# Optimization experiments

Hardware: AMD Instinct MI355X
Metric: run time of the kernel (lower is better)

Reference implementation:

```python
import jax, jax.numpy as jnp
import numpy as np

BATCH = 8
IMG = 224
PATCH = 16
IN_CH = 8
D_MODEL = 768
DEPTH = 4
D_INNER = 2 * D_MODEL          # 1536
D_STATE = 16
DT_RANK = D_MODEL // 16        # 48
D_CONV = 4
NUM_CLASSES = 1000
EPS = 1e-5


def setup_inputs() -> dict:
    key = jax.random.key(0)
    ks = jax.random.split(key, 16)
    g = lambda i, shape, s=0.02: jax.random.normal(ks[i], shape, jnp.float32) * s
    L = DEPTH
    inp = {}
    inp['x'] = jax.random.normal(ks[0], (BATCH, IN_CH, IMG, IMG), jnp.float32)
    # patch embed: Conv3d(1, D, (1,p,p)) == shared 2D conv applied to every channel
    inp['patch_w'] = g(1, (D_MODEL, PATCH, PATCH))
    inp['patch_b'] = jnp.zeros((D_MODEL,), jnp.float32)
    inp['channel_embed'] = g(2, (IN_CH, D_MODEL))
    # per-block params (stacked over depth)
    inp['norm_w'] = jnp.ones((L, D_MODEL), jnp.float32)
    inp['norm_b'] = jnp.zeros((L, D_MODEL), jnp.float32)
    inp['in_proj_w'] = g(3, (L, 2 * D_INNER, D_MODEL))
    inp['conv_w'] = g(4, (L, D_INNER, D_CONV), 0.1)
    inp['conv_b'] = jnp.zeros((L, D_INNER), jnp.float32)
    inp['x_proj_w'] = g(5, (L, DT_RANK + 2 * D_STATE, D_INNER))
    inp['dt_proj_w'] = g(6, (L, D_INNER, DT_RANK), 0.1)
    inp['dt_proj_b'] = jnp.full((L, D_INNER), -4.6, jnp.float32)  # softplus^-1(0.01)
    inp['A_log'] = jnp.tile(jnp.log(jnp.arange(1, D_STATE + 1, dtype=jnp.float32)), (L, D_INNER, 1))
    inp['D_param'] = jnp.ones((L, D_INNER), jnp.float32)
    inp['ssm_norm_w'] = jnp.ones((L, D_INNER), jnp.float32)
    inp['ssm_norm_b'] = jnp.zeros((L, D_INNER), jnp.float32)
    inp['out_proj_w'] = g(7, (L, D_MODEL, D_INNER), 0.02 / np.sqrt(L))
    # final norm + classification head
    inp['norm_f_w'] = jnp.ones((D_MODEL,), jnp.float32)
    inp['norm_f_b'] = jnp.zeros((D_MODEL,), jnp.float32)
    inp['head_w'] = g(8, (NUM_CLASSES, D_MODEL))
    inp['head_b'] = jnp.zeros((NUM_CLASSES,), jnp.float32)
    return inp


def _ln(x, w, b):
    mu = x.mean(-1, keepdims=True)
    var = ((x - mu) ** 2).mean(-1, keepdims=True)
    return (x - mu) * jax.lax.rsqrt(var + EPS) * w + b


def _silu(x):
    return x * jax.nn.sigmoid(x)


def _mamba(h, ipw, cw, cb, xpw, dtw, dtb, Alog, Dp, snw, snb, opw):
    # h: [B, L, D_MODEL]
    B, Lseq, _ = h.shape
    xz = jnp.einsum('bld,ed->ble', h, ipw)               # [B, L, 2*di]
    x, z = jnp.split(xz, 2, axis=-1)
    # causal depthwise conv1d along L (kernel D_CONV)
    xp = jnp.pad(x, ((0, 0), (D_CONV - 1, 0), (0, 0)))
    xc = cb + sum(xp[:, k:k + Lseq, :] * cw[:, k] for k in range(D_CONV))
    x = _silu(xc)
    dbc = jnp.einsum('bld,ed->ble', x, xpw)              # [B, L, dt_rank+2N]
    dt_r = dbc[..., :DT_RANK]
    Bm = dbc[..., DT_RANK:DT_RANK + D_STATE]
    Cm = dbc[..., DT_RANK + D_STATE:]
    dt = jax.nn.softplus(jnp.einsum('blr,dr->bld', dt_r, dtw) + dtb)  # [B, L, di]
    A = -jnp.exp(Alog)                                    # [di, N]

    def step(hstate, t):
        dt_t, B_t, C_t, x_t = t                           # [B,di],[B,N],[B,N],[B,di]
        dA = jnp.exp(dt_t[..., None] * A)                 # [B, di, N]
        hstate = dA * hstate + (dt_t * x_t)[..., None] * B_t[:, None, :]
        y = jnp.einsum('bdn,bn->bd', hstate, C_t)
        return hstate, y

    h0 = jnp.zeros((B, D_INNER, D_STATE), x.dtype)
    xs = (dt.transpose(1, 0, 2), Bm.transpose(1, 0, 2),
          Cm.transpose(1, 0, 2), x.transpose(1, 0, 2))
    _, ys = jax.lax.scan(step, h0, xs)                    # [L, B, di]
    y = ys.transpose(1, 0, 2) + Dp * x
    y = _ln(y, snw, snb)                                  # norm-after-SSM
    y = y * _silu(z)
    return jnp.einsum('ble,de->bld', y, opw)


def reference(x, patch_w, patch_b, channel_embed, norm_w, norm_b, in_proj_w,
              conv_w, conv_b, x_proj_w, dt_proj_w, dt_proj_b, A_log, D_param,
              ssm_norm_w, ssm_norm_b, out_proj_w, norm_f_w, norm_f_b,
              head_w, head_b):
    B, C, H, W = x.shape
    hg, wg = H // PATCH, W // PATCH
    # shared-filter patch embed per channel: [B,C,hg,wg,D]
    xp = x.reshape(B, C, hg, PATCH, wg, PATCH)
    emb = jnp.einsum('bchpwq,dpq->bchwd', xp, patch_w) + patch_b
    emb = emb + channel_embed[None, :, None, None, :]
    # Channel-First scan order -> token order (h, w, C): [B, hg*wg*C, D]
    tok = emb.transpose(0, 2, 3, 1, 4).reshape(B, hg * wg * C, D_MODEL)

    hidden, residual = tok, None
    for i in range(DEPTH):
        residual = hidden if residual is None else residual + hidden
        hn = _ln(residual, norm_w[i], norm_b[i])
        hidden = _mamba(hn, in_proj_w[i], conv_w[i], conv_b[i], x_proj_w[i],
                        dt_proj_w[i], dt_proj_b[i], A_log[i], D_param[i],
                        ssm_norm_w[i], ssm_norm_b[i], out_proj_w[i])
    residual = residual + hidden
    hf = _ln(residual, norm_f_w, norm_f_b)
    pooled = hf.mean(axis=1)                              # mean pooling head
    return pooled @ head_w.T + head_b
```

## Files before the change

### kernel.cpp

```cpp
#include <hip/hip_runtime.h>
#include <hip/hip_bf16.h>

typedef __hip_bfloat16 bf16;
typedef __attribute__((ext_vector_type(8))) short short8;
typedef __attribute__((ext_vector_type(4))) float float4v;

#define BATCH 8
#define SEQ   1568
#define M_TOK (BATCH*SEQ)
#define DM    768
#define DI    1536
#define XZW   3072
#define DS    16
#define DTR   48
#define NCLS  1000
#define LAYERS 4
#define CHUNK 112
#define NCH   14
#define DBCW  128

__device__ __forceinline__ float b2f(bf16 v){ return __bfloat162float(v); }
__device__ __forceinline__ bf16  f2b(float v){ return __float2bfloat16(v); }
__device__ __forceinline__ float us2f(unsigned short u){
    unsigned v = ((unsigned)u) << 16; float f; __builtin_memcpy(&f, &v, 4); return f;
}
__device__ __forceinline__ void gload_lds16(const void* g, void* l){
    __builtin_amdgcn_global_load_lds(
        (const __attribute__((address_space(1))) void*)g,
        (__attribute__((address_space(3))) void*)l, 16, 0, 0);
}
template<int CTRL>
__device__ __forceinline__ float dpp_add(float p){
    int pi; __builtin_memcpy(&pi, &p, 4);
    int mi = __builtin_amdgcn_update_dpp(pi, pi, CTRL, 0xF, 0xF, false);
    float m; __builtin_memcpy(&m, &mi, 4);
    return p + m;
}

__global__ void detect_dtype(const unsigned short* __restrict__ probe, unsigned* __restrict__ flag)
{
    if (threadIdx.x == 0 && blockIdx.x == 0) flag[0] = (probe[0] == 0) ? 1u : 0u;
}

struct CvtArgs {
    const void* src[21];
    void*       dst[21];
    int         n[21];
    unsigned    f32mask;
    int         total;
};

__global__ __launch_bounds__(256)
void convert_all(CvtArgs a, const unsigned* __restrict__ flag)
{
    int idx = blockIdx.x*256 + threadIdx.x;
    if (idx >= a.total) return;
    int i = 0, base = 0;
    while (idx >= base + a.n[i]) { base += a.n[i]; ++i; }
    int j = idx - base;
    bool in_f32 = flag[0] != 0;
    if ((a.f32mask >> i) & 1u) {
        float v = in_f32 ? ((const float*)a.src[i])[j] : b2f(((const bf16*)a.src[i])[j]);
        ((float*)a.dst[i])[j] = v;
    } else {
        bf16 v = in_f32 ? f2b(((const float*)a.src[i])[j]) : ((const bf16*)a.src[i])[j];
        ((bf16*)a.dst[i])[j] = v;
    }
}

__global__ __launch_bounds__(256)
void pad_dtw(const bf16* __restrict__ src, bf16* __restrict__ dst)
{
    int idx = blockIdx.x*256 + threadIdx.x;
    if (idx >= LAYERS*DI*64) return;
    int l = idx / (DI*64);
    int d = (idx / 64) % DI;
    int c = idx % 64;
    dst[idx] = (c < DTR) ? src[((size_t)l*DI + d)*DTR + c] : f2b(0.f);
}

__global__ __launch_bounds__(256)
void gather_patches(const bf16* __restrict__ x, bf16* __restrict__ Ap, int b0)
{
    size_t idx = (size_t)blockIdx.x*256 + threadIdx.x;
    int i = (int)(idx & 255);
    int m = (int)(idx >> 8);
    int b = b0 + m / SEQ, s = m % SEQ;
    int hw = s >> 3, c = s & 7;
    int h = hw / 14, w = hw % 14;
    int p = i >> 4, q = i & 15;
    Ap[idx] = x[(((size_t)(b*8 + c)*224) + h*16 + p)*224 + w*16 + q];
}

__global__ __launch_bounds__(256)
void gemm_mfma(const bf16* __restrict__ A, int lda,
               const bf16* __restrict__ W, int ldw,
               float* __restrict__ Cf, bf16* __restrict__ Cb, int ldc,
               const float* __restrict__ bias, const float* __restrict__ chan,
               int M, int N, int K, int epi)
{
    __shared__ short As[128*40];
    __shared__ short Bs[128*40];
    int tid  = threadIdx.x;
    int m0   = blockIdx.x*128, n0 = blockIdx.y*128;
    int lane = tid & 63, wv = tid >> 6;
    int wm = (wv >> 1)*64, wn = (wv & 1)*64;
    int l15 = lane & 15, quad = lane >> 4;

    float4v acc[4][4];
    #pragma unroll
    for (int i = 0; i < 4; ++i)
        #pragma unroll
        for (int j = 0; j < 4; ++j) acc[i][j] = (float4v){0.f,0.f,0.f,0.f};

    const short8 zv8 = {0,0,0,0,0,0,0,0};
    for (int k0 = 0; k0 < K; k0 += 32) {
        #pragma unroll
        for (int u = 0; u < 2; ++u) {
            int c   = tid*2 + u;
            int row = c >> 2, ch = c & 3;
            bool kok = (k0 + ch*8 + 8) <= K;
            short8 va = (kok && m0 + row < M)
                ? *(const short8*)((const short*)A + (size_t)(m0+row)*lda + k0 + ch*8) : zv8;
            *(short8*)(As + row*40 + ch*8) = va;
            short8 vb = (kok && n0 + row < N)
                ? *(const short8*)((const short*)W + (size_t)(n0+row)*ldw + k0 + ch*8) : zv8;
            *(short8*)(Bs + row*40 + ch*8) = vb;
        }
        __syncthreads();
        short8 av[4], bv[4];
        #pragma unroll
        for (int i = 0; i < 4; ++i) av[i] = *(const short8*)(As + (wm + i*16 + l15)*40 + quad*8);
        #pragma unroll
        for (int j = 0; j < 4; ++j) bv[j] = *(const short8*)(Bs + (wn + j*16 + l15)*40 + quad*8);
        #pragma unroll
        for (int i = 0; i < 4; ++i)
            #pragma unroll
            for (int j = 0; j < 4; ++j)
                acc[i][j] = __builtin_amdgcn_mfma_f32_16x16x32_bf16(av[i], bv[j], acc[i][j], 0, 0, 0);
        __syncthreads();
    }

    #pragma unroll
    for (int i = 0; i < 4; ++i) {
        #pragma unroll
        for (int j = 0; j < 4; ++j) {
            int gn = n0 + wn + j*16 + l15;
            if (gn >= N) continue;
            #pragma unroll
            for (int r = 0; r < 4; ++r) {
                int gm = m0 + wm + i*16 + quad*4 + r;
                if (gm >= M) continue;
                float v = acc[i][j][r];
                size_t off = (size_t)gm*ldc + gn;
                if (epi == 0)      Cb[off] = f2b(v);
                else if (epi == 1) {
                    v += bias[gn];
                    v = (v > 20.f) ? v : log1pf(__expf(v));
                    Cb[off] = f2b(v);
                }
                else if (epi == 2) Cf[off] += v;
                else               Cf[off] = v + bias[gn] + chan[(size_t)(gm & 7)*N + gn];
            }
        }
    }
}

__global__ __launch_bounds__(256)
void gemm_mfma_fast(const bf16* __restrict__ A, int lda,
                    const bf16* __restrict__ W, int ldw,
                    float* __restrict__ Cf, bf16* __restrict__ Cb, int ldc,
                    const float* __restrict__ bias, const float* __restrict__ chan,
                    int N, int K, int epi)
{
    __shared__ short As[128*32];
    __shared__ short Bs[128*32];
    int tid  = threadIdx.x;
    int m0   = blockIdx.x*128, n0 = blockIdx.y*128;
    int lane = tid & 63, wv = tid >> 6;
    int wm = (wv >> 1)*64, wn = (wv & 1)*64;
    int l15 = lane & 15, quad = lane >> 4;

    int srow = (lane >> 2);
    int skof = (lane & 3) * 8;

    float4v acc[4][4];
    #pragma unroll
    for (int i = 0; i < 4; ++i)
        #pragma unroll
        for (int j = 0; j < 4; ++j) acc[i][j] = (float4v){0.f,0.f,0.f,0.f};

    const short* Ab = (const short*)A;
    const short* Wb = (const short*)W;

    for (int k0 = 0; k0 < K; k0 += 32) {
        #pragma unroll
        for (int u = 0; u < 2; ++u) {
            int c = wv*2 + u;
            int row = c*16 + srow;
            gload_lds16(Ab + (size_t)(m0+row)*lda + k0 + skof, As + c*512);
            gload_lds16(Wb + (size_t)(n0+row)*ldw + k0 + skof, Bs + c*512);
        }
        __syncthreads();
        short8 av[4], bv[4];
        #pragma unroll
        for (int i = 0; i < 4; ++i) av[i] = *(const short8*)(As + (wm + i*16 + l15)*32 + quad*8);
        #pragma unroll
        for (int j = 0; j < 4; ++j) bv[j] = *(const short8*)(Bs + (wn + j*16 + l15)*32 + quad*8);
        #pragma unroll
        for (int i = 0; i < 4; ++i)
            #pragma unroll
            for (int j = 0; j < 4; ++j)
                acc[i][j] = __builtin_amdgcn_mfma_f32_16x16x32_bf16(av[i], bv[j], acc[i][j], 0, 0, 0);
        __syncthreads();
    }

    #pragma unroll
    for (int i = 0; i < 4; ++i) {
        #pragma unroll
        for (int j = 0; j < 4; ++j) {
            int gn = n0 + wn + j*16 + l15;
            #pragma unroll
            for (int r = 0; r < 4; ++r) {
                int gm = m0 + wm + i*16 + quad*4 + r;
                float v = acc[i][j][r];
                size_t off = (size_t)gm*ldc + gn;
                if (epi == 0)      Cb[off] = f2b(v);
                else if (epi == 1) {
                    v += bias[gn];
                    v = (v > 20.f) ? v : log1pf(__expf(v));
                    Cb[off] = f2b(v);
                }
                else if (epi == 2) Cf[off] += v;
                else               Cf[off] = v + bias[gn] + chan[(size_t)(gm & 7)*N + gn];
            }
        }
    }
}

__global__ __launch_bounds__(256)
void ln768(const float* __restrict__ X, const float* __restrict__ w,
           const float* __restrict__ bb, bf16* __restrict__ out)
{
    __shared__ float red[8];
    size_t t = blockIdx.x;
    const float* x = X + t*DM;
    float v[3]; float s = 0.f, s2 = 0.f;
    #pragma unroll
    for (int r = 0; r < 3; ++r) {
        v[r] = x[threadIdx.x + 256*r];
        s += v[r]; s2 += v[r]*v[r];
    }
    #pragma unroll
    for (int o = 32; o; o >>= 1) { s += __shfl_down(s, o, 64); s2 += __shfl_down(s2, o, 64); }
    if ((threadIdx.x & 63) == 0) { red[threadIdx.x >> 6] = s; red[(threadIdx.x >> 6) + 4] = s2; }
    __syncthreads();
    s  = red[0]+red[1]+red[2]+red[3];
    s2 = red[4]+red[5]+red[6]+red[7];
    float mu  = s * (1.f/DM);
    float inv = rsqrtf(fmaxf(s2*(1.f/DM) - mu*mu, 0.f) + 1e-5f);
    #pragma unroll
    for (int r = 0; r < 3; ++r) {
        int i = threadIdx.x + 256*r;
        out[t*DM + i] = f2b((v[r]-mu)*inv*w[i] + bb[i]);
    }
}

__global__ __launch_bounds__(256)
void conv_silu(const bf16* __restrict__ xz, const float* __restrict__ cw,
               const float* __restrict__ cb, bf16* __restrict__ xc)
{
    size_t idx = (size_t)blockIdx.x*256 + threadIdx.x;
    int dv = (int)(idx % (DI/8));
    int m  = (int)(idx / (DI/8));
    int b = m / SEQ, t = m % SEQ;
    int d = dv*8;

    float4v cwq[8];
    #pragma unroll
    for (int j = 0; j < 8; ++j) cwq[j] = *(const float4v*)(cw + (size_t)(d+j)*4);

    float acc[8];
    #pragma unroll
    for (int j = 0; j < 8; ++j) acc[j] = cb[d+j];

    #pragma unroll
    for (int k = 0; k < 4; ++k) {
        int tt = t + k - 3;
        if (tt >= 0) {
            short8 v = *(const short8*)((const short*)xz + (size_t)(b*SEQ + tt)*XZW + d);
            #pragma unroll
            for (int j = 0; j < 8; ++j)
                acc[j] += us2f((unsigned short)v[j]) * cwq[j][k];
        }
    }
    short8 o;
    #pragma unroll
    for (int j = 0; j < 8; ++j) {
        float sig = 1.f/(1.f + __expf(-acc[j]));
        bf16 r = f2b(acc[j]*sig);
        unsigned short u; __builtin_memcpy(&u, &r, 2); o[j] = (short)u;
    }
    *(short8*)((short*)xc + idx*8) = o;
}


__global__ __launch_bounds__(256)
void scan_pass1(const bf16* __restrict__ dt, const bf16* __restrict__ x,
                const bf16* __restrict__ dbc, const float* __restrict__ Alog,
                float* __restrict__ hend, float* __restrict__ Pprod, int nin2)
{
    __shared__ float dtT[2][64][20], xT[2][64][20];
    __shared__ float BsT[2][16][16];
    int c  = blockIdx.x / nin2;
    int r  = blockIdx.x % nin2;
    int b  = r / 24;
    int d0 = (r % 24) * 64;
    int tid = threadIdx.x;
    int sq = tid & 3;
    int dl = tid >> 2;
    int d  = d0 + dl;

    float4v Aq = *(const float4v*)(Alog + (size_t)d*DS + sq*4);
    float A2[4], h[4];
    #pragma unroll
    for (int k = 0; k < 4; ++k) { A2[k] = -__expf(Aq[k]) * 1.44269504f; h[k] = 0.f; }
    float sdt = 0.f;

    int js = tid >> 4, dg = tid & 15;
    bool doB = tid < 64;
    int j2 = tid >> 2;

    const unsigned short* pdt = (const unsigned short*)dt + ((size_t)b*SEQ + js)*DI + d0 + dg*4;
    const unsigned short* px  = (const unsigned short*)x  + ((size_t)b*SEQ + js)*DI + d0 + dg*4;
    const unsigned short* pbc = (const unsigned short*)dbc + ((size_t)b*SEQ + (j2 & 15))*DBCW + DTR + sq*4;
    int tbase = c * CHUNK;
    const int NT = CHUNK/16;

    ushort4 vdt, vx, vbc;
    auto stage = [&](int buf){
        dtT[buf][dg*4+0][js] = us2f(vdt.x); dtT[buf][dg*4+1][js] = us2f(vdt.y);
        dtT[buf][dg*4+2][js] = us2f(vdt.z); dtT[buf][dg*4+3][js] = us2f(vdt.w);
        xT [buf][dg*4+0][js] = us2f(vx.x);  xT [buf][dg*4+1][js] = us2f(vx.y);
        xT [buf][dg*4+2][js] = us2f(vx.z);  xT [buf][dg*4+3][js] = us2f(vx.w);
        if (doB)
            *(float4v*)&BsT[buf][j2][sq*4] =
                (float4v){us2f(vbc.x), us2f(vbc.y), us2f(vbc.z), us2f(vbc.w)};
    };
    auto fetch = [&](int T){
        vdt = *(const ushort4*)(pdt + (size_t)(tbase + T*16)*DI);
        vx  = *(const ushort4*)(px  + (size_t)(tbase + T*16)*DI);
        if (doB) vbc = *(const ushort4*)(pbc + (size_t)(tbase + T*16)*DBCW);
    };

    fetch(0); stage(0); fetch(1);
    __syncthreads();

    for (int t = 0; t < NT; ++t) {
        int cur = t & 1;
        if (t+1 < NT) stage(cur^1);
        if (t+2 < NT) fetch(t+2);
        #pragma unroll
        for (int jj = 0; jj < 16; jj += 4) {
            float4v dtq = *(const float4v*)&dtT[cur][dl][jj];
            float4v xq  = *(const float4v*)&xT [cur][dl][jj];
            #pragma unroll
            for (int k2 = 0; k2 < 4; ++k2) {
                float dtv = dtq[k2];
                float dtx = dtv * xq[k2];
                float4v Bq = *(const float4v*)&BsT[cur][jj+k2][sq*4];
                #pragma unroll
                for (int k = 0; k < 4; ++k)
                    h[k] = exp2f(dtv*A2[k])*h[k] + dtx*Bq[k];
                sdt += dtv;
            }
        }
        __syncthreads();
    }
    size_t o = (((size_t)c*nin2 + r)*256 + tid)*4;
    *(float4v*)(hend + o) = (float4v){h[0], h[1], h[2], h[3]};
    *(float4v*)(Pprod + o) = (float4v){exp2f(A2[0]*sdt), exp2f(A2[1]*sdt),
                                       exp2f(A2[2]*sdt), exp2f(A2[3]*sdt)};
}

__global__ __launch_bounds__(256)
void scan_mid(const float* __restrict__ hend, const float* __restrict__ Pprod,
              float* __restrict__ hstart, int nin2)
{
    int r = blockIdx.x, tid = threadIdx.x;
    float4v h = (float4v){0.f,0.f,0.f,0.f};
    *(float4v*)(hstart + ((size_t)r*256 + tid)*4) = h;
    for (int c = 1; c < NCH; ++c) {
        size_t p = (((size_t)(c-1)*nin2 + r)*256 + tid)*4;
        float4v P  = *(const float4v*)(Pprod + p);
        float4v he = *(const float4v*)(hend + p);
        h = P*h + he;
        *(float4v*)(hstart + (((size_t)c*nin2 + r)*256 + tid)*4) = h;
    }
}

__global__ __launch_bounds__(256)
void scan_pass2(const bf16* __restrict__ dt, const bf16* __restrict__ x,
                const bf16* __restrict__ dbc, const float* __restrict__ Alog,
                const float* __restrict__ Dpar, const float* __restrict__ hstart,
                bf16* __restrict__ y, int nin2)
{
    __shared__ float dtT[2][64][20], xT[2][64][20];
    __shared__ float BsT[2][16][16], CsT[2][16][16];
    __shared__ bf16  ys[16][64];
    int c  = blockIdx.x / nin2;
    int r  = blockIdx.x % nin2;
    int b  = r / 24;
    int d0 = (r % 24) * 64;
    int tid = threadIdx.x;
    int sq = tid & 3;
    int dl = tid >> 2;
    int d  = d0 + dl;

    float4v Aq = *(const float4v*)(Alog + (size_t)d*DS + sq*4);
    float A2[4], h[4];
    {
        float4v h0 = *(const float4v*)(hstart + (((size_t)c*nin2 + r)*256 + tid)*4);
        #pragma unroll
        for (int k = 0; k < 4; ++k) { A2[k] = -__expf(Aq[k]) * 1.44269504f; h[k] = h0[k]; }
    }
    float Dv = Dpar[d];

    int js = tid >> 4, dg = tid & 15;
    bool doBC = tid < 128;
    int j2 = (tid & 63) >> 2;

    const unsigned short* pdt = (const unsigned short*)dt + ((size_t)b*SEQ + js)*DI + d0 + dg*4;
    const unsigned short* px  = (const unsigned short*)x  + ((size_t)b*SEQ + js)*DI + d0 + dg*4;
    const unsigned short* pbc = (const unsigned short*)dbc + ((size_t)b*SEQ + j2)*DBCW + DTR
                                + ((tid >= 64) ? DS : 0) + sq*4;
    float* bc0 = (tid < 64) ? &BsT[0][j2][sq*4] : &CsT[0][j2][sq*4];
    int tbase = c * CHUNK;
    const int NT = CHUNK/16;

    ushort4 vdt, vx, vbc;
    auto stage = [&](int buf){
        dtT[buf][dg*4+0][js] = us2f(vdt.x); dtT[buf][dg*4+1][js] = us2f(vdt.y);
        dtT[buf][dg*4+2][js] = us2f(vdt.z); dtT[buf][dg*4+3][js] = us2f(vdt.w);
        xT [buf][dg*4+0][js] = us2f(vx.x);  xT [buf][dg*4+1][js] = us2f(vx.y);
        xT [buf][dg*4+2][js] = us2f(vx.z);  xT [buf][dg*4+3][js] = us2f(vx.w);
        if (doBC)
            *(float4v*)(bc0 + (size_t)buf*256) =
                (float4v){us2f(vbc.x), us2f(vbc.y), us2f(vbc.z), us2f(vbc.w)};
    };
    auto fetch = [&](int T){
        vdt = *(const ushort4*)(pdt + (size_t)(tbase + T*16)*DI);
        vx  = *(const ushort4*)(px  + (size_t)(tbase + T*16)*DI);
        if (doBC) vbc = *(const ushort4*)(pbc + (size_t)(tbase + T*16)*DBCW);
    };

    fetch(0); stage(0); fetch(1);
    __syncthreads();

    for (int t = 0; t < NT; ++t) {
        int cur = t & 1;
        if (t+1 < NT) stage(cur^1);
        if (t+2 < NT) fetch(t+2);

        #pragma unroll
        for (int jj = 0; jj < 16; jj += 4) {
            float4v dtq = *(const float4v*)&dtT[cur][dl][jj];
            float4v xq  = *(const float4v*)&xT [cur][dl][jj];
            #pragma unroll
            for (int k2 = 0; k2 < 4; ++k2) {
                float dtv = dtq[k2];
                float xv  = xq[k2];
                float dtx = dtv * xv;
                float4v Bq = *(const float4v*)&BsT[cur][jj+k2][sq*4];
                float4v Cq = *(const float4v*)&CsT[cur][jj+k2][sq*4];
                float p = 0.f;
                #pragma unroll
                for (int k = 0; k < 4; ++k) {
                    h[k] = exp2f(dtv*A2[k])*h[k] + dtx*Bq[k];
                    p += h[k]*Cq[k];
                }
                p = dpp_add<0xB1>(p);
                p = dpp_add<0x4E>(p);
                if (sq == 0) ys[jj+k2][dl] = f2b(p + Dv*xv);
            }
        }
        __syncthreads();
        {
            size_t rowm = (size_t)(b*SEQ + tbase + t*16 + js);
            ushort4 vy = *(const ushort4*)((const unsigned short*)&ys[js][0] + dg*4);
            *(ushort4*)((unsigned short*)y + rowm*XZW + d0 + dg*4) = vy;
        }
        __syncthreads();
    }
}

__global__ __launch_bounds__(192)
void gate_ln(const bf16* __restrict__ xz,
             const float* __restrict__ w, const float* __restrict__ bb,
             bf16* __restrict__ out)
{
    __shared__ float red[6];
    size_t t = blockIdx.x;
    int tid = threadIdx.x;
    int i0 = tid*8;
    short8 y8 = *(const short8*)((const short*)xz + t*XZW + i0);
    short8 z8 = *(const short8*)((const short*)xz + t*XZW + DI + i0);
    float vy[8];
    float s = 0.f, s2 = 0.f;
    #pragma unroll
    for (int j = 0; j < 8; ++j) {
        vy[j] = us2f((unsigned short)y8[j]);
        s += vy[j]; s2 += vy[j]*vy[j];
    }
    #pragma unroll
    for (int o = 32; o; o >>= 1) { s += __shfl_down(s, o, 64); s2 += __shfl_down(s2, o, 64); }
    if ((tid & 63) == 0) { red[tid >> 6] = s; red[(tid >> 6) + 3] = s2; }
    __syncthreads();
    s  = red[0]+red[1]+red[2];
    s2 = red[3]+red[4]+red[5];
    float mu  = s * (1.f/DI);
    float inv = rsqrtf(fmaxf(s2*(1.f/DI) - mu*mu, 0.f) + 1e-5f);
    float4v w0 = *(const float4v*)(w + i0);
    float4v w1 = *(const float4v*)(w + i0 + 4);
    float4v b0 = *(const float4v*)(bb + i0);
    float4v b1 = *(const float4v*)(bb + i0 + 4);
    short8 o8;
    #pragma unroll
    for (int j = 0; j < 8; ++j) {
        float zv = us2f((unsigned short)z8[j]);
        float sig = 1.f/(1.f + __expf(-zv));
        float wj = (j < 4) ? w0[j] : w1[j-4];
        float bj = (j < 4) ? b0[j] : b1[j-4];
        bf16 rr = f2b(((vy[j]-mu)*inv*wj + bj) * (zv*sig));
        unsigned short u; __builtin_memcpy(&u, &rr, 2); o8[j] = (short)u;
    }
    *(short8*)((short*)out + t*DI + i0) = o8;
}

__global__ __launch_bounds__(256)
void pool_partial(const bf16* __restrict__ hf, float* __restrict__ part)
{
    int blk = blockIdx.x;
    int b = blk / NCH, c = blk % NCH;
    int tid = threadIdx.x;
    const bf16* p = hf + ((size_t)b*SEQ + c*CHUNK)*DM;
    float s0 = 0.f, s1 = 0.f, s2 = 0.f;
    for (int t = 0; t < CHUNK; ++t) {
        s0 += b2f(p[(size_t)t*DM + tid]);
        s1 += b2f(p[(size_t)t*DM + tid + 256]);
        s2 += b2f(p[(size_t)t*DM + tid + 512]);
    }
    part[(size_t)blk*DM + tid]       = s0;
    part[(size_t)blk*DM + tid + 256] = s1;
    part[(size_t)blk*DM + tid + 512] = s2;
}

__global__ __launch_bounds__(256)
void pool_finish(const float* __restrict__ part, float* __restrict__ pooled)
{
    int idx = blockIdx.x*256 + threadIdx.x;
    int b = idx / DM, dm = idx % DM;
    float s = 0.f;
    for (int c = 0; c < NCH; ++c) s += part[((size_t)b*NCH + c)*DM + dm];
    pooled[idx] = s * (1.f/SEQ);
}

__global__ __launch_bounds__(256)
void head_kernel(const unsigned* __restrict__ flag,
                 const float* __restrict__ pooled, const bf16* __restrict__ hw,
                 const float* __restrict__ hb, void* __restrict__ out)
{
    int idx = blockIdx.x*256 + threadIdx.x;
    if (idx >= BATCH*NCLS) return;
    int b = idx & 7, n = idx >> 3;
    const float* p = pooled + b*DM;
    const unsigned short* w = (const unsigned short*)hw + (size_t)n*DM;
    float acc = hb[n];
    for (int k = 0; k < DM; k += 4) {
        ushort4 wv = *(const ushort4*)(w + k);
        acc += p[k]*us2f(wv.x) + p[k+1]*us2f(wv.y) + p[k+2]*us2f(wv.z) + p[k+3]*us2f(wv.w);
    }
    int o = b*NCLS + n;
    if (flag[0]) ((float*)out)[o] = acc;
    else         ((bf16*)out)[o]  = f2b(acc);
}

extern "C" void kernel_launch(void* const* d_in, const int* in_sizes, int n_in,
                              void* d_out, int out_size, void* d_ws, size_t ws_size,
                              hipStream_t stream)
{
    (void)n_in; (void)out_size;
    dim3 blk(256);

    const bool is_f32[21] = { false, false, true, true, true, true, false, true, true,
                              false, false, true,  true, true, true, true, false,
                              true,  true,  false, true };

    size_t off = 0;
    auto carve = [&](size_t bytes) -> void* {
        void* q = (char*)d_ws + off;
        off += (bytes + 255) & ~(size_t)255;
        return q;
    };

    unsigned* flag = (unsigned*)carve(256);
    void* canon[21];
    for (int i = 0; i < 21; ++i)
        canon[i] = carve((size_t)in_sizes[i] * (is_f32[i] ? 4 : 2));

    float* residual = (float*)carve((size_t)M_TOK*DM*4);
    bf16*  hn       = (bf16*) carve((size_t)M_TOK*DM*2);
    float* pooled   = (float*)carve((size_t)BATCH*DM*4);
    float* poolpart = (float*)carve((size_t)BATCH*NCH*DM*4);
    bf16*  dtw_pad  = (bf16*) carve((size_t)LAYERS*DI*64*2);

    const size_t scanbuf1 = (size_t)NCH*96*256*4;
    const size_t inner1 = (((size_t)SEQ*XZW*2 + 255) & ~(size_t)255)
                          + 2*(((size_t)SEQ*DI*2 + 255) & ~(size_t)255)
                          + (((size_t)SEQ*DBCW*2 + 255) & ~(size_t)255)
                          + 3*((scanbuf1 + 255) & ~(size_t)255);
    int g = 8;
    while (g > 1 && off + (size_t)g*inner1 > ws_size) g >>= 1;

    bf16* xz  = (bf16*)carve((size_t)g*SEQ*XZW*2);
    bf16* xc  = (bf16*)carve((size_t)g*SEQ*DI*2);
    bf16* dtb = (bf16*)carve((size_t)g*SEQ*DI*2);
    bf16* dbc = (bf16*)carve((size_t)g*SEQ*DBCW*2);
    float* hend   = (float*)carve((size_t)g*scanbuf1);
    float* Pprod  = (float*)carve((size_t)g*scanbuf1);
    float* hstart = (float*)carve((size_t)g*scanbuf1);
    bf16* Ap    = xz;
    bf16* gated = dtb;

    detect_dtype<<<1, 64, 0, stream>>>((const unsigned short*)d_in[4], flag);

    {
        int order[21];
        for (int i = 0; i < 21; ++i) order[i] = i;
        for (int a = 0; a < 21; ++a)
            for (int b2 = a+1; b2 < 21; ++b2)
                if (in_sizes[order[b2]] > in_sizes[order[a]]) {
                    int tmp = order[a]; order[a] = order[b2]; order[b2] = tmp;
                }
        CvtArgs ca;
        ca.f32mask = 0; ca.total = 0;
        for (int k = 0; k < 21; ++k) {
            int i = order[k];
            ca.src[k] = d_in[i];
            ca.dst[k] = canon[i];
            ca.n[k]   = in_sizes[i];
            ca.total += in_sizes[i];
            if (is_f32[i]) ca.f32mask |= (1u << k);
        }
        convert_all<<<(ca.total + 255)/256, blk, 0, stream>>>(ca, flag);
    }

    const bf16*  xin   = (const bf16*) canon[0];
    const bf16*  pw    = (const bf16*) canon[1];
    const float* pb    = (const float*)canon[2];
    const float* chan  = (const float*)canon[3];
    const float* nw    = (const float*)canon[4];
    const float* nb    = (const float*)canon[5];
    const bf16*  ipw   = (const bf16*) canon[6];
    const float* cw    = (const float*)canon[7];
    const float* cb    = (const float*)canon[8];
    const bf16*  xpw   = (const bf16*) canon[9];
    const bf16*  dtw   = (const bf16*) canon[10];
    const float* dtbia = (const float*)canon[11];
    const float* Alog  = (const float*)canon[12];
    const float* Dpar  = (const float*)canon[13];
    const float* snw   = (const float*)canon[14];
    const float* snb   = (const float*)canon[15];
    const bf16*  opw   = (const bf16*) canon[16];
    const float* nfw   = (const float*)canon[17];
    const float* nfb   = (const float*)canon[18];
    const bf16*  hw    = (const bf16*) canon[19];
    const float* hb    = (const float*)canon[20];

    pad_dtw<<<(LAYERS*DI*64 + 255)/256, blk, 0, stream>>>(dtw, dtw_pad);

    const int MG  = g*SEQ;
    const int nin2 = g*24;

    auto launch_gemm = [&](const bf16* A, int lda, const bf16* W, int ldw,
                           float* Cf, bf16* Cb, int ldc,
                           const float* bias, const float* chan_,
                           int M, int N, int K, int epi) {
        dim3 gr((M + 127)/128, (N + 127)/128);
        bool clean = (M & 127) == 0 && (N & 127) == 0 && (K & 31) == 0;
        if (clean && gr.x*gr.y >= 192)
            gemm_mfma_fast<<<gr, blk, 0, stream>>>(A, lda, W, ldw, Cf, Cb, ldc,
                                                   bias, chan_, N, K, epi);
        else
            gemm_mfma<<<gr, blk, 0, stream>>>(A, lda, W, ldw, Cf, Cb, ldc,
                                              bias, chan_, M, N, K, epi);
    };

    for (int b0 = 0; b0 < BATCH; b0 += g) {
        gather_patches<<<MG, blk, 0, stream>>>(xin, Ap, b0);
        launch_gemm(Ap, 256, pw, 256,
                    residual + (size_t)b0*SEQ*DM, nullptr, DM,
                    pb, chan, MG, DM, 256, 3);
    }

    for (int l = 0; l < LAYERS; ++l) {
        ln768<<<M_TOK, blk, 0, stream>>>(residual, nw + l*DM, nb + l*DM, hn);
        for (int b0 = 0; b0 < BATCH; b0 += g) {
            const bf16* hng = hn + (size_t)b0*SEQ*DM;
            launch_gemm(hng, DM, ipw + (size_t)l*2*DI*DM, DM,
                        nullptr, xz, XZW, nullptr, nullptr, MG, 2*DI, DM, 0);
            conv_silu<<<(MG*(DI/8))/256, blk, 0, stream>>>(xz, cw + (size_t)l*DI*4, cb + l*DI, xc);
            launch_gemm(xc, DI, xpw + (size_t)l*80*DI, DI,
                        nullptr, dbc, DBCW, nullptr, nullptr, MG, 80, DI, 0);
            launch_gemm(dbc, DBCW, dtw_pad + (size_t)l*DI*64, 64,
                        nullptr, dtb, DI, dtbia + l*DI, nullptr, MG, DI, 64, 1);
            scan_pass1<<<(NCH-1)*nin2, blk, 0, stream>>>(dtb, xc, dbc,
                                                         Alog + (size_t)l*DI*DS,
                                                         hend, Pprod, nin2);
            scan_mid<<<nin2, blk, 0, stream>>>(hend, Pprod, hstart, nin2);
            scan_pass2<<<NCH*nin2, blk, 0, stream>>>(dtb, xc, dbc,
                                                     Alog + (size_t)l*DI*DS,
                                                     Dpar + l*DI, hstart, xz, nin2);
            gate_ln<<<MG, dim3(192), 0, stream>>>(xz, snw + l*DI, snb + l*DI, gated);
            launch_gemm(gated, DI, opw + (size_t)l*DM*DI, DI,
                        residual + (size_t)b0*SEQ*DM, nullptr, DM,
                        nullptr, nullptr, MG, DM, DI, 2);
        }
    }

    ln768<<<M_TOK, blk, 0, stream>>>(residual, nfw, nfb, hn);
    pool_partial<<<BATCH*NCH, blk, 0, stream>>>(hn, poolpart);
    pool_finish<<<(BATCH*DM)/256, blk, 0, stream>>>(poolpart, pooled);
    head_kernel<<<(BATCH*NCLS + 255)/256, blk, 0, stream>>>(flag, pooled, hw, hb, d_out);
}
```

Baseline: 3.396 ms.

## Split-K the x_proj GEMM into two halves and vectorize the input conversion kernel

```diff
diff --git a/kernel.cpp b/kernel.cpp
--- a/kernel.cpp
+++ b/kernel.cpp
@@ -24,6 +24,9 @@
 __device__ __forceinline__ float us2f(unsigned short u){
     unsigned v = ((unsigned)u) << 16; float f; __builtin_memcpy(&f, &v, 4); return f;
 }
+__device__ __forceinline__ short f2bs(float v){
+    bf16 r = f2b(v); unsigned short u; __builtin_memcpy(&u, &r, 2); return (short)u;
+}
 __device__ __forceinline__ void gload_lds16(const void* g, void* l){
     __builtin_amdgcn_global_load_lds(
         (const __attribute__((address_space(1))) void*)g,
@@ -46,25 +49,55 @@
     const void* src[21];
     void*       dst[21];
     int         n[21];
+    int         n8[21];
     unsigned    f32mask;
-    int         total;
+    int         total8;
 };
 
 __global__ __launch_bounds__(256)
-void convert_all(CvtArgs a, const unsigned* __restrict__ flag)
-{
-    int idx = blockIdx.x*256 + threadIdx.x;
-    if (idx >= a.total) return;
+void convert_all8(CvtArgs a, const unsigned* __restrict__ flag)
+{
+    int g8 = blockIdx.x*256 + threadIdx.x;
+    if (g8 >= a.total8) return;
     int i = 0, base = 0;
-    while (idx >= base + a.n[i]) { base += a.n[i]; ++i; }
-    int j = idx - base;
-    bool in_f32 = flag[0] != 0;
-    if ((a.f32mask >> i) & 1u) {
-        float v = in_f32 ? ((const float*)a.src[i])[j] : b2f(((const bf16*)a.src[i])[j]);
-        ((float*)a.dst[i])[j] = v;
+    while (g8 >= base + a.n8[i]) { base += a.n8[i]; ++i; }
+    int j = (g8 - base)*8;
+    bool in_f32  = flag[0] != 0;
+    bool out_f32 = (a.f32mask >> i) & 1u;
+    if (j + 8 <= a.n[i]) {
+        if (in_f32) {
+            float4v v0 = *(const float4v*)((const float*)a.src[i] + j);
+            float4v v1 = *(const float4v*)((const float*)a.src[i] + j + 4);
+            if (out_f32) {
+                *(float4v*)((float*)a.dst[i] + j)     = v0;
+                *(float4v*)((float*)a.dst[i] + j + 4) = v1;
+            } else {
+                short8 o;
+                #pragma unroll
+                for (int k = 0; k < 4; ++k) { o[k] = f2bs(v0[k]); o[k+4] = f2bs(v1[k]); }
+                *(short8*)((short*)a.dst[i] + j) = o;
+            }
+        } else {
+            short8 v = *(const short8*)((const short*)a.src[i] + j);
+            if (out_f32) {
+                float4v v0, v1;
+                #pragma unroll
+                for (int k = 0; k < 4; ++k) {
+                    v0[k] = us2f((unsigned short)v[k]);
+                    v1[k] = us2f((unsigned short)v[k+4]);
+                }
+                *(float4v*)((float*)a.dst[i] + j)     = v0;
+                *(float4v*)((float*)a.dst[i] + j + 4) = v1;
+            } else {
+                *(short8*)((short*)a.dst[i] + j) = v;
+            }
+        }
     } else {
-        bf16 v = in_f32 ? f2b(((const float*)a.src[i])[j]) : ((const bf16*)a.src[i])[j];
-        ((bf16*)a.dst[i])[j] = v;
+        for (int q = j; q < a.n[i]; ++q) {
+            float v = in_f32 ? ((const float*)a.src[i])[q] : b2f(((const bf16*)a.src[i])[q]);
+            if (out_f32) ((float*)a.dst[i])[q] = v;
+            else         ((bf16*) a.dst[i])[q] = f2b(v);
+        }
     }
 }
 
@@ -101,6 +134,8 @@
 {
     __shared__ short As[128*40];
     __shared__ short Bs[128*40];
+    int kb = blockIdx.z * K;
+    A += kb;  W += kb;
     int tid  = threadIdx.x;
     int m0   = blockIdx.x*128, n0 = blockIdx.y*128;
     int lane = tid & 63, wv = tid >> 6;
@@ -160,10 +195,27 @@
                     Cb[off] = f2b(v);
                 }
                 else if (epi == 2) Cf[off] += v;
+                else if (epi == 5) Cf[(size_t)blockIdx.z*((size_t)M*ldc) + off] = v;
                 else               Cf[off] = v + bias[gn] + chan[(size_t)(gm & 7)*N + gn];
             }
         }
     }
+}
+
+__global__ __launch_bounds__(256)
+void dbc_combine(const float* __restrict__ dbcf, bf16* __restrict__ dbc, int MG)
+{
+    int idx = blockIdx.x*256 + threadIdx.x;
+    if (idx >= MG*20) return;
+    int m = idx / 20, c4 = (idx % 20)*4;
+    float4v a = *(const float4v*)(dbcf + (size_t)m*80 + c4);
+    float4v b = *(const float4v*)(dbcf + (size_t)MG*80 + (size_t)m*80 + c4);
+    ushort4 o;
+    o.x = (unsigned short)f2bs(a[0] + b[0]);
+    o.y = (unsigned short)f2bs(a[1] + b[1]);
+    o.z = (unsigned short)f2bs(a[2] + b[2]);
+    o.w = (unsigned short)f2bs(a[3] + b[3]);
+    *(ushort4*)((unsigned short*)dbc + (size_t)m*DBCW + c4) = o;
 }
 
 __global__ __launch_bounds__(256)
@@ -298,8 +350,7 @@
     #pragma unroll
     for (int j = 0; j < 8; ++j) {
         float sig = 1.f/(1.f + __expf(-acc[j]));
-        bf16 r = f2b(acc[j]*sig);
-        unsigned short u; __builtin_memcpy(&u, &r, 2); o[j] = (short)u;
+        o[j] = f2bs(acc[j]*sig);
     }
     *(short8*)((short*)xc + idx*8) = o;
 }
@@ -531,8 +582,7 @@
         float sig = 1.f/(1.f + __expf(-zv));
         float wj = (j < 4) ? w0[j] : w1[j-4];
         float bj = (j < 4) ? b0[j] : b1[j-4];
-        bf16 rr = f2b(((vy[j]-mu)*inv*wj + bj) * (zv*sig));
-        unsigned short u; __builtin_memcpy(&u, &rr, 2); o8[j] = (short)u;
+        o8[j] = f2bs(((vy[j]-mu)*inv*wj + bj) * (zv*sig));
     }
     *(short8*)((short*)out + t*DI + i0) = o8;
 }
@@ -618,6 +668,7 @@
     const size_t inner1 = (((size_t)SEQ*XZW*2 + 255) & ~(size_t)255)
                           + 2*(((size_t)SEQ*DI*2 + 255) & ~(size_t)255)
                           + (((size_t)SEQ*DBCW*2 + 255) & ~(size_t)255)
+                          + 2*(((size_t)SEQ*80*4 + 255) & ~(size_t)255)
                           + 3*((scanbuf1 + 255) & ~(size_t)255);
     int g = 8;
     while (g > 1 && off + (size_t)g*inner1 > ws_size) g >>= 1;
@@ -626,6 +677,7 @@
     bf16* xc  = (bf16*)carve((size_t)g*SEQ*DI*2);
     bf16* dtb = (bf16*)carve((size_t)g*SEQ*DI*2);
     bf16* dbc = (bf16*)carve((size_t)g*SEQ*DBCW*2);
+    float* dbcf = (float*)carve((size_t)g*SEQ*80*4*2);
     float* hend   = (float*)carve((size_t)g*scanbuf1);
     float* Pprod  = (float*)carve((size_t)g*scanbuf1);
     float* hstart = (float*)carve((size_t)g*scanbuf1);
@@ -643,16 +695,17 @@
                     int tmp = order[a]; order[a] = order[b2]; order[b2] = tmp;
                 }
         CvtArgs ca;
-        ca.f32mask = 0; ca.total = 0;
+        ca.f32mask = 0; ca.total8 = 0;
         for (int k = 0; k < 21; ++k) {
             int i = order[k];
             ca.src[k] = d_in[i];
             ca.dst[k] = canon[i];
             ca.n[k]   = in_sizes[i];
-            ca.total += in_sizes[i];
+            ca.n8[k]  = (in_sizes[i] + 7)/8;
+            ca.total8 += ca.n8[k];
             if (is_f32[i]) ca.f32mask |= (1u << k);
         }
-        convert_all<<<(ca.total + 255)/256, blk, 0, stream>>>(ca, flag);
+        convert_all8<<<(ca.total8 + 255)/256, blk, 0, stream>>>(ca, flag);
     }
 
     const bf16*  xin   = (const bf16*) canon[0];
@@ -710,8 +763,13 @@
             launch_gemm(hng, DM, ipw + (size_t)l*2*DI*DM, DM,
                         nullptr, xz, XZW, nullptr, nullptr, MG, 2*DI, DM, 0);
             conv_silu<<<(MG*(DI/8))/256, blk, 0, stream>>>(xz, cw + (size_t)l*DI*4, cb + l*DI, xc);
-            launch_gemm(xc, DI, xpw + (size_t)l*80*DI, DI,
-                        nullptr, dbc, DBCW, nullptr, nullptr, MG, 80, DI, 0);
+            {
+                dim3 gr((MG + 127)/128, 1, 2);
+                gemm_mfma<<<gr, blk, 0, stream>>>(xc, DI, xpw + (size_t)l*80*DI, DI,
+                                                  dbcf, nullptr, 80, nullptr, nullptr,
+                                                  MG, 80, DI/2, 5);
+                dbc_combine<<<(MG*20 + 255)/256, blk, 0, stream>>>(dbcf, dbc, MG);
+            }
             launch_gemm(dbc, DBCW, dtw_pad + (size_t)l*DI*64, 64,
                         nullptr, dtb, DI, dtbia + l*DI, nullptr, MG, DI, 64, 1);
             scan_pass1<<<(NCH-1)*nin2, blk, 0, stream>>>(dtb, xc, dbc,
```

After: 3.509 ms, median of 2. +3.3%, slower.
